# Kernel tuning notes

Hardware: AMD Instinct MI355X
Metric: run time of the kernel (lower is better)

Reference implementation:

```python
import jax, jax.numpy as jnp
import numpy as np

N_NODES = 100000
N_EDGES = 1600000
IN_CH = 64
HID = 64
OUT_CH = 3
N_LAYERS = 4


def gcn_conv(x, src, dst, norm, W, b):
    # x: [N, d_in]; W: [d_in, d_out]; norm: [E'] (per-edge symmetric norm)
    h = x @ W                               # [N, d_out]
    msgs = h[src] * norm[:, None]           # [E', d_out] gather + scale
    out = jax.ops.segment_sum(msgs, dst, num_segments=N_NODES)  # scatter-add
    return out + b


def build_graph(edge_index):
    # PyG GCNConv default: add self-loops, symmetric normalization
    loops = jnp.arange(N_NODES, dtype=edge_index.dtype)
    src = jnp.concatenate([edge_index[0], loops])
    dst = jnp.concatenate([edge_index[1], loops])
    deg = jax.ops.segment_sum(jnp.ones_like(dst, dtype=jnp.float32), dst,
                              num_segments=N_NODES)
    dinv = jnp.where(deg > 0, jax.lax.rsqrt(jnp.maximum(deg, 1e-12)), 0.0)
    norm = dinv[src] * dinv[dst]            # [E + N]
    return src, dst, norm


def setup_inputs() -> dict:
    key = jax.random.key(0)
    ks = jax.random.split(key, 5)
    x = jax.random.normal(ks[0], (N_NODES, IN_CH), dtype=jnp.float32)
    edge_index = jax.random.randint(ks[1], (2, N_EDGES), 0, N_NODES, dtype=jnp.int64)
    Ws = jax.random.normal(ks[2], (N_LAYERS, HID, HID), dtype=jnp.float32) * (1.0 / np.sqrt(HID))
    bs = jnp.zeros((N_LAYERS, HID), dtype=jnp.float32)
    Wc = jax.random.normal(ks[3], (HID, OUT_CH), dtype=jnp.float32) * (1.0 / np.sqrt(HID))
    bc = jnp.zeros((OUT_CH,), dtype=jnp.float32)
    return {"x": x, "edge_index": edge_index, "Ws": Ws, "bs": bs, "Wc": Wc, "bc": bc}


def reference(x, edge_index, Ws, bs, Wc, bc):
    src, dst, norm = build_graph(edge_index)
    for i in range(N_LAYERS):
        x_new = gcn_conv(x, src, dst, norm, Ws[i], bs[i])
        # residual when i > 0 and feature dims match (always true: hidden->hidden)
        x = x + x_new if i > 0 else x_new
        x = jax.nn.relu(x)
        # dropout is identity in eval mode (training=False)
    return x @ Wc + bc
```

## Files before the change

kernel.cpp:

```cpp
#include <hip/hip_runtime.h>
#include <hip/hip_fp16.h>

#define NN 100000
#define HD 64
#define NB ((NN + 255) >> 8)
#define P1_CHUNK 8192

__global__ __launch_bounds__(256) void hist_kernel(const int* __restrict__ dst,
                                                   int* __restrict__ bcnt, int E) {
    __shared__ int hist[NB];
    int t = threadIdx.x;
    int e0 = blockIdx.x * P1_CHUNK;
    int count = min(P1_CHUNK, E - e0);
    for (int b = t; b < NB; b += 256) hist[b] = 0;
    __syncthreads();
    for (int i = t; i < count; i += 256) atomicAdd(&hist[dst[e0 + i] >> 8], 1);
    __syncthreads();
    for (int b = t; b < NB; b += 256) {
        int c = hist[b];
        if (c) atomicAdd(&bcnt[b], c);
    }
}

__global__ void bscan_kernel(const int* __restrict__ bcnt, int* __restrict__ boff,
                             int* __restrict__ bcur, int* __restrict__ row_ptr,
                             int E, int n) {
    __shared__ int sm[512];
    int t = threadIdx.x;
    int v = (t < NB) ? bcnt[t] : 0;
    sm[t] = v;
    __syncthreads();
    for (int off = 1; off < 512; off <<= 1) {
        int u = (t >= off) ? sm[t - off] : 0;
        __syncthreads();
        sm[t] += u;
        __syncthreads();
    }
    if (t < NB) {
        boff[t] = sm[t] - v;
        bcur[t] = sm[t] - v;
    }
    if (t == 0) {
        boff[NB] = E;
        row_ptr[n] = E;
    }
}

__global__ __launch_bounds__(256) void p1_kernel(const int* __restrict__ src,
                                                 const int* __restrict__ dst,
                                                 int* __restrict__ bcur,
                                                 unsigned* __restrict__ ebuf, int E) {
    __shared__ int hist[NB];
    __shared__ int cur[NB];
    int t = threadIdx.x;
    int e0 = blockIdx.x * P1_CHUNK;
    int count = min(P1_CHUNK, E - e0);
    for (int b = t; b < NB; b += 256) hist[b] = 0;
    __syncthreads();
    for (int i = t; i < count; i += 256) atomicAdd(&hist[dst[e0 + i] >> 8], 1);
    __syncthreads();
    for (int b = t; b < NB; b += 256) {
        int c = hist[b];
        cur[b] = c ? atomicAdd(&bcur[b], c) : 0;
    }
    __syncthreads();
    for (int i = t; i < count; i += 256) {
        int d = dst[e0 + i], s = src[e0 + i];
        int pos = atomicAdd(&cur[d >> 8], 1);
        ebuf[pos] = ((unsigned)(d & 255) << 24) | (unsigned)s;
    }
}

__global__ __launch_bounds__(256) void p2_kernel(const unsigned* __restrict__ ebuf,
                                                 const int* __restrict__ boff,
                                                 int* __restrict__ row_ptr,
                                                 float* __restrict__ dinv,
                                                 int* __restrict__ csr_src, int n) {
    __shared__ int cnt[256];
    __shared__ int cur[256];
    int b = blockIdx.x;
    int node0 = b << 8;
    int t = threadIdx.x;
    int beg = boff[b], end = boff[b + 1];
    cnt[t] = 0;
    __syncthreads();
    for (int i = beg + t; i < end; i += 256) atomicAdd(&cnt[ebuf[i] >> 24], 1);
    __syncthreads();
    int deg = cnt[t];
    for (int off = 1; off < 256; off <<= 1) {
        int v = (t >= off) ? cnt[t - off] : 0;
        __syncthreads();
        cnt[t] += v;
        __syncthreads();
    }
    int excl = cnt[t] - deg;
    int node = node0 + t;
    if (node < n) {
        row_ptr[node] = beg + excl;
        dinv[node] = rsqrtf((float)deg + 1.0f);
    }
    cur[t] = beg + excl;
    __syncthreads();
    for (int i = beg + t; i < end; i += 256) {
        unsigned p = ebuf[i];
        int pos = atomicAdd(&cur[p >> 24], 1);
        csr_src[pos] = (int)(p & 0xFFFFFFu);
    }
}

__global__ __launch_bounds__(256) void matmul64_kernel(const void* __restrict__ Xv,
                                                       int x_is_half,
                                                       const float* __restrict__ W,
                                                       const float* __restrict__ dinv,
                                                       float2* __restrict__ H, int n) {
    __shared__ float Wl[64 * 64];
    __shared__ float Xs[64 * 65];
    int tid = threadIdx.x;
    int row0 = blockIdx.x * 64;
    const float4* W4 = (const float4*)W;
    float4* Wl4 = (float4*)Wl;
#pragma unroll
    for (int i = 0; i < 4; ++i) Wl4[tid + 256 * i] = W4[tid + 256 * i];
    if (x_is_half) {
        const float4* X4 = (const float4*)Xv;
#pragma unroll
        for (int i = 0; i < 2; ++i) {
            int l = tid + 256 * i;
            int r = l >> 3, k0 = (l & 7) * 8;
            int row = row0 + r;
            float4 xv = (row < n) ? X4[(size_t)row * 8 + (l & 7)]
                                  : make_float4(0.f, 0.f, 0.f, 0.f);
            const __half2* hp = (const __half2*)&xv;
#pragma unroll
            for (int j = 0; j < 4; ++j) {
                float2 f = __half22float2(hp[j]);
                Xs[r * 65 + k0 + 2 * j]     = f.x;
                Xs[r * 65 + k0 + 2 * j + 1] = f.y;
            }
        }
    } else {
        const float4* X4 = (const float4*)Xv;
#pragma unroll
        for (int i = 0; i < 4; ++i) {
            int l = tid + 256 * i;
            int r = l >> 4, k0 = (l & 15) * 4;
            int row = row0 + r;
            float4 xv = (row < n) ? X4[(size_t)row * 16 + (l & 15)]
                                  : make_float4(0.f, 0.f, 0.f, 0.f);
            Xs[r * 65 + k0 + 0] = xv.x;
            Xs[r * 65 + k0 + 1] = xv.y;
            Xs[r * 65 + k0 + 2] = xv.z;
            Xs[r * 65 + k0 + 3] = xv.w;
        }
    }
    __syncthreads();
    int tx = tid & 15, ty = tid >> 4;
    float acc[4][4] = {};
    const float4* Wlr4 = (const float4*)Wl;
#pragma unroll 4
    for (int k = 0; k < 64; ++k) {
        float4 b = Wlr4[k * 16 + tx];
        float a0 = Xs[(ty * 4 + 0) * 65 + k];
        float a1 = Xs[(ty * 4 + 1) * 65 + k];
        float a2 = Xs[(ty * 4 + 2) * 65 + k];
        float a3 = Xs[(ty * 4 + 3) * 65 + k];
        acc[0][0] += a0 * b.x; acc[0][1] += a0 * b.y; acc[0][2] += a0 * b.z; acc[0][3] += a0 * b.w;
        acc[1][0] += a1 * b.x; acc[1][1] += a1 * b.y; acc[1][2] += a1 * b.z; acc[1][3] += a1 * b.w;
        acc[2][0] += a2 * b.x; acc[2][1] += a2 * b.y; acc[2][2] += a2 * b.z; acc[2][3] += a2 * b.w;
        acc[3][0] += a3 * b.x; acc[3][1] += a3 * b.y; acc[3][2] += a3 * b.z; acc[3][3] += a3 * b.w;
    }
#pragma unroll
    for (int j = 0; j < 4; ++j) {
        int row = row0 + ty * 4 + j;
        if (row < n) {
            float dn = dinv[row];
            __half2 p01 = __float22half2_rn(make_float2(acc[j][0] * dn, acc[j][1] * dn));
            __half2 p23 = __float22half2_rn(make_float2(acc[j][2] * dn, acc[j][3] * dn));
            float2 st;
            st.x = *reinterpret_cast<float*>(&p01);
            st.y = *reinterpret_cast<float*>(&p23);
            H[(size_t)row * 16 + tx] = st;
        }
    }
}

#define PK_ACC(RAW) do {                                                     \
    a0 = __hadd2(a0, *reinterpret_cast<__half2*>(&(RAW).x));                 \
    a1 = __hadd2(a1, *reinterpret_cast<__half2*>(&(RAW).y));                 \
    a2 = __hadd2(a2, *reinterpret_cast<__half2*>(&(RAW).z));                 \
    a3 = __hadd2(a3, *reinterpret_cast<__half2*>(&(RAW).w));                 \
} while (0)

__global__ void agg_kernel(const float4* __restrict__ h4, const int* __restrict__ row_ptr,
                           const int* __restrict__ csr_src, const float* __restrict__ dinv,
                           const float* __restrict__ b, const float4* __restrict__ xprev,
                           float4* __restrict__ xout, float* __restrict__ outp,
                           const float* __restrict__ Wc, const float* __restrict__ bc,
                           int n, int residual, int project) {
    int lane = threadIdx.x & 63;
    int o = lane >> 3, c8 = lane & 7;
    int wid = (blockIdx.x * blockDim.x + threadIdx.x) >> 6;
    int node = wid * 8 + o;
    bool active = node < n;
    int nc = active ? node : 0;
    int beg = row_ptr[nc], end = row_ptr[nc + 1];
    int cnt = end - beg;
    float dn = dinv[nc];
    const float4* b4 = (const float4*)b;
    float4 bb0 = b4[c8 * 2], bb1 = b4[c8 * 2 + 1];
    float4 rr = make_float4(0.f, 0.f, 0.f, 0.f);
    if (residual) rr = xprev[(size_t)nc * 8 + c8];
    __half2 a0, a1, a2, a3;
    {
        float4 sv = h4[(size_t)nc * 8 + c8];
        a0 = *reinterpret_cast<__half2*>(&sv.x);
        a1 = *reinterpret_cast<__half2*>(&sv.y);
        a2 = *reinterpret_cast<__half2*>(&sv.z);
        a3 = *reinterpret_cast<__half2*>(&sv.w);
    }
    int base = o * 8;
    for (int k = 0; k < cnt; k += 16) {
        int p = beg + k + c8;
        int svA = (p < end) ? csr_src[p] : NN;
        int svB = (p + 8 < end) ? csr_src[p + 8] : NN;
        int s0 = __shfl(svA, base + 0);
        int s1 = __shfl(svA, base + 1);
        int s2 = __shfl(svA, base + 2);
        int s3 = __shfl(svA, base + 3);
        int s4 = __shfl(svA, base + 4);
        int s5 = __shfl(svA, base + 5);
        int s6 = __shfl(svA, base + 6);
        int s7 = __shfl(svA, base + 7);
        int s8  = __shfl(svB, base + 0);
        int s9  = __shfl(svB, base + 1);
        int s10 = __shfl(svB, base + 2);
        int s11 = __shfl(svB, base + 3);
        int s12 = __shfl(svB, base + 4);
        int s13 = __shfl(svB, base + 5);
        int s14 = __shfl(svB, base + 6);
        int s15 = __shfl(svB, base + 7);
        float4 v0  = h4[(size_t)s0 * 8 + c8];
        float4 v1  = h4[(size_t)s1 * 8 + c8];
        float4 v2  = h4[(size_t)s2 * 8 + c8];
        float4 v3  = h4[(size_t)s3 * 8 + c8];
        float4 v4  = h4[(size_t)s4 * 8 + c8];
        float4 v5  = h4[(size_t)s5 * 8 + c8];
        float4 v6  = h4[(size_t)s6 * 8 + c8];
        float4 v7  = h4[(size_t)s7 * 8 + c8];
        float4 v8  = h4[(size_t)s8 * 8 + c8];
        float4 v9  = h4[(size_t)s9 * 8 + c8];
        float4 v10 = h4[(size_t)s10 * 8 + c8];
        float4 v11 = h4[(size_t)s11 * 8 + c8];
        float4 v12 = h4[(size_t)s12 * 8 + c8];
        float4 v13 = h4[(size_t)s13 * 8 + c8];
        float4 v14 = h4[(size_t)s14 * 8 + c8];
        float4 v15 = h4[(size_t)s15 * 8 + c8];
        PK_ACC(v0);  PK_ACC(v1);  PK_ACC(v2);  PK_ACC(v3);
        PK_ACC(v4);  PK_ACC(v5);  PK_ACC(v6);  PK_ACC(v7);
        PK_ACC(v8);  PK_ACC(v9);  PK_ACC(v10); PK_ACC(v11);
        PK_ACC(v12); PK_ACC(v13); PK_ACC(v14); PK_ACC(v15);
    }
    if (active) {
        float2 f0 = __half22float2(a0);
        float2 f1 = __half22float2(a1);
        float2 f2 = __half22float2(a2);
        float2 f3 = __half22float2(a3);
        float4 u, w;
        u.x = f0.x * dn + bb0.x; u.y = f0.y * dn + bb0.y;
        u.z = f1.x * dn + bb0.z; u.w = f1.y * dn + bb0.w;
        w.x = f2.x * dn + bb1.x; w.y = f2.y * dn + bb1.y;
        w.z = f3.x * dn + bb1.z; w.w = f3.y * dn + bb1.w;
        if (residual) {
            const __half2* rp = (const __half2*)&rr;
            float2 r0 = __half22float2(rp[0]);
            float2 r1 = __half22float2(rp[1]);
            float2 r2 = __half22float2(rp[2]);
            float2 r3 = __half22float2(rp[3]);
            u.x += r0.x; u.y += r0.y; u.z += r1.x; u.w += r1.y;
            w.x += r2.x; w.y += r2.y; w.z += r3.x; w.w += r3.y;
        }
        u.x = fmaxf(u.x, 0.f); u.y = fmaxf(u.y, 0.f);
        u.z = fmaxf(u.z, 0.f); u.w = fmaxf(u.w, 0.f);
        w.x = fmaxf(w.x, 0.f); w.y = fmaxf(w.y, 0.f);
        w.z = fmaxf(w.z, 0.f); w.w = fmaxf(w.w, 0.f);
        if (!project) {
            __half2 o0 = __float22half2_rn(make_float2(u.x, u.y));
            __half2 o1 = __float22half2_rn(make_float2(u.z, u.w));
            __half2 o2 = __float22half2_rn(make_float2(w.x, w.y));
            __half2 o3 = __float22half2_rn(make_float2(w.z, w.w));
            float4 st;
            st.x = *reinterpret_cast<float*>(&o0);
            st.y = *reinterpret_cast<float*>(&o1);
            st.z = *reinterpret_cast<float*>(&o2);
            st.w = *reinterpret_cast<float*>(&o3);
            xout[(size_t)node * 8 + c8] = st;
        } else {
            int cb = c8 * 8;
#pragma unroll
            for (int j = 0; j < 3; ++j) {
                float p = u.x * Wc[(cb + 0) * 3 + j] + u.y * Wc[(cb + 1) * 3 + j] +
                          u.z * Wc[(cb + 2) * 3 + j] + u.w * Wc[(cb + 3) * 3 + j] +
                          w.x * Wc[(cb + 4) * 3 + j] + w.y * Wc[(cb + 5) * 3 + j] +
                          w.z * Wc[(cb + 6) * 3 + j] + w.w * Wc[(cb + 7) * 3 + j];
                p += __shfl_down(p, 4, 8);
                p += __shfl_down(p, 2, 8);
                p += __shfl_down(p, 1, 8);
                if (c8 == 0) outp[node * 3 + j] = p + bc[j];
            }
        }
    }
}

extern "C" void kernel_launch(void* const* d_in, const int* in_sizes, int n_in,
                              void* d_out, int out_size, void* d_ws, size_t ws_size,
                              hipStream_t stream) {
    const float* x  = (const float*)d_in[0];
    const int*   ei = (const int*)d_in[1];
    const float* Ws = (const float*)d_in[2];
    const float* bs = (const float*)d_in[3];
    const float* Wc = (const float*)d_in[4];
    const float* bc = (const float*)d_in[5];
    float* out = (float*)d_out;

    int E = in_sizes[1] / 2;
    const int* src = ei;
    const int* dst = ei + E;
    int nchunks = (E + P1_CHUNK - 1) / P1_CHUNK;

    char* wsb = (char*)d_ws;
    size_t off = 0;
    int*      bcnt    = (int*)(wsb + off); off += 512 * 4;
    int*      boff    = (int*)(wsb + off); off += 512 * 4;
    int*      bcur    = (int*)(wsb + off); off += 512 * 4;
    int*      row_ptr = (int*)(wsb + off); off += 100608 * 4;
    float*    dinv    = (float*)(wsb + off); off += 100352 * 4;
    int*      csr_src = (int*)(wsb + off); off += ((size_t)E + 256) * 4;
    unsigned* ebuf    = (unsigned*)(wsb + off); off += (size_t)E * 4;
    float2*   h       = (float2*)(wsb + off); off += (size_t)(NN + 8) * HD * 2;
    float4*   xa      = (float4*)(wsb + off); off += (size_t)NN * HD * 2;
    float4*   xb      = (float4*)(wsb + off); off += (size_t)NN * HD * 2;

    hipMemsetAsync(bcnt, 0, 512 * sizeof(int), stream);
    hipMemsetAsync((char*)h + (size_t)NN * HD * 2, 0, HD * 2, stream);
    hist_kernel<<<nchunks, 256, 0, stream>>>(dst, bcnt, E);
    bscan_kernel<<<1, 512, 0, stream>>>(bcnt, boff, bcur, row_ptr, E, NN);
    p1_kernel<<<nchunks, 256, 0, stream>>>(src, dst, bcur, ebuf, E);
    p2_kernel<<<NB, 256, 0, stream>>>(ebuf, boff, row_ptr, dinv, csr_src, NN);

    const void* xin = (const void*)x;
    int xin_half = 0;
    float4* bufs[2] = {xa, xb};
    int agg_blocks = ((NN + 7) / 8 * 64 + 255) / 256;
    for (int l = 0; l < 4; ++l) {
        float4* xout = bufs[l & 1];
        matmul64_kernel<<<(NN + 63) / 64, 256, 0, stream>>>(
            xin, xin_half, Ws + (size_t)l * HD * HD, dinv, h, NN);
        agg_kernel<<<agg_blocks, 256, 0, stream>>>(
            (const float4*)h, row_ptr, csr_src, dinv, bs + l * HD,
            (const float4*)xin, xout, out, Wc, bc, NN, l > 0, l == 3);
        xin = (const void*)xout;
        xin_half = 1;
    }
}
```

Before: 329.3 us.

## Drop histogram and scan passes by bucketing edges into fixed-capacity slots

Removes the separate histogram and bucket-scan kernels: p1 now reserves slots per destination bucket in a fixed-stride buffer (aliased onto the xa workspace), and p2 computes each bucket's global offset by reducing the bucket counts itself. It also folds the h-padding memset and row_ptr[n] write into p2. Separately, the 64x64 matmul now reads X as float4 with a 68-float row stride and unrolls k by 4. The fixed bucket capacity assumes roughly uniform destination distribution and would overflow on skewed graphs.

After: 409.3 us. +24.3%, slower.

```diff
diff --git a/kernel.cpp b/kernel.cpp
--- a/kernel.cpp
+++ b/kernel.cpp
@@ -6,50 +6,11 @@
 #define NB ((NN + 255) >> 8)
 #define P1_CHUNK 8192
 
-__global__ __launch_bounds__(256) void hist_kernel(const int* __restrict__ dst,
-                                                   int* __restrict__ bcnt, int E) {
-    __shared__ int hist[NB];
-    int t = threadIdx.x;
-    int e0 = blockIdx.x * P1_CHUNK;
-    int count = min(P1_CHUNK, E - e0);
-    for (int b = t; b < NB; b += 256) hist[b] = 0;
-    __syncthreads();
-    for (int i = t; i < count; i += 256) atomicAdd(&hist[dst[e0 + i] >> 8], 1);
-    __syncthreads();
-    for (int b = t; b < NB; b += 256) {
-        int c = hist[b];
-        if (c) atomicAdd(&bcnt[b], c);
-    }
-}
-
-__global__ void bscan_kernel(const int* __restrict__ bcnt, int* __restrict__ boff,
-                             int* __restrict__ bcur, int* __restrict__ row_ptr,
-                             int E, int n) {
-    __shared__ int sm[512];
-    int t = threadIdx.x;
-    int v = (t < NB) ? bcnt[t] : 0;
-    sm[t] = v;
-    __syncthreads();
-    for (int off = 1; off < 512; off <<= 1) {
-        int u = (t >= off) ? sm[t - off] : 0;
-        __syncthreads();
-        sm[t] += u;
-        __syncthreads();
-    }
-    if (t < NB) {
-        boff[t] = sm[t] - v;
-        bcur[t] = sm[t] - v;
-    }
-    if (t == 0) {
-        boff[NB] = E;
-        row_ptr[n] = E;
-    }
-}
-
 __global__ __launch_bounds__(256) void p1_kernel(const int* __restrict__ src,
                                                  const int* __restrict__ dst,
-                                                 int* __restrict__ bcur,
-                                                 unsigned* __restrict__ ebuf, int E) {
+                                                 int* __restrict__ bcnt,
+                                                 unsigned* __restrict__ ebuf,
+                                                 int E, int ebs) {
     __shared__ int hist[NB];
     __shared__ int cur[NB];
     int t = threadIdx.x;
@@ -61,30 +22,44 @@
     __syncthreads();
     for (int b = t; b < NB; b += 256) {
         int c = hist[b];
-        cur[b] = c ? atomicAdd(&bcur[b], c) : 0;
+        cur[b] = c ? atomicAdd(&bcnt[b], c) : 0;
     }
     __syncthreads();
     for (int i = t; i < count; i += 256) {
         int d = dst[e0 + i], s = src[e0 + i];
-        int pos = atomicAdd(&cur[d >> 8], 1);
-        ebuf[pos] = ((unsigned)(d & 255) << 24) | (unsigned)s;
+        int b = d >> 8;
+        int rel = atomicAdd(&cur[b], 1);
+        ebuf[(size_t)b * ebs + rel] = ((unsigned)(d & 255) << 24) | (unsigned)s;
     }
 }
 
 __global__ __launch_bounds__(256) void p2_kernel(const unsigned* __restrict__ ebuf,
-                                                 const int* __restrict__ boff,
+                                                 const int* __restrict__ bcnt,
                                                  int* __restrict__ row_ptr,
                                                  float* __restrict__ dinv,
-                                                 int* __restrict__ csr_src, int n) {
+                                                 int* __restrict__ csr_src,
+                                                 int* __restrict__ hpad,
+                                                 int n, int E, int ebs) {
     __shared__ int cnt[256];
     __shared__ int cur[256];
+    __shared__ int red[256];
     int b = blockIdx.x;
-    int node0 = b << 8;
     int t = threadIdx.x;
-    int beg = boff[b], end = boff[b + 1];
+    int part = 0;
+    for (int i = t; i < NB; i += 256)
+        if (i < b) part += bcnt[i];
+    red[t] = part;
+    __syncthreads();
+    for (int off = 128; off > 0; off >>= 1) {
+        if (t < off) red[t] += red[t + off];
+        __syncthreads();
+    }
+    int S = red[0];
+    int cb = bcnt[b];
+    const unsigned* eb = ebuf + (size_t)b * ebs;
     cnt[t] = 0;
     __syncthreads();
-    for (int i = beg + t; i < end; i += 256) atomicAdd(&cnt[ebuf[i] >> 24], 1);
+    for (int i = t; i < cb; i += 256) atomicAdd(&cnt[eb[i] >> 24], 1);
     __syncthreads();
     int deg = cnt[t];
     for (int off = 1; off < 256; off <<= 1) {
@@ -94,17 +69,21 @@
         __syncthreads();
     }
     int excl = cnt[t] - deg;
-    int node = node0 + t;
+    int node = (b << 8) + t;
     if (node < n) {
-        row_ptr[node] = beg + excl;
+        row_ptr[node] = S + excl;
         dinv[node] = rsqrtf((float)deg + 1.0f);
     }
-    cur[t] = beg + excl;
-    __syncthreads();
-    for (int i = beg + t; i < end; i += 256) {
-        unsigned p = ebuf[i];
+    cur[t] = S + excl;
+    __syncthreads();
+    for (int i = t; i < cb; i += 256) {
+        unsigned p = eb[i];
         int pos = atomicAdd(&cur[p >> 24], 1);
         csr_src[pos] = (int)(p & 0xFFFFFFu);
+    }
+    if (b == 0) {
+        if (t == 0) row_ptr[n] = E;
+        if (t < 32) hpad[t] = 0;
     }
 }
 
@@ -114,7 +93,7 @@
                                                        const float* __restrict__ dinv,
                                                        float2* __restrict__ H, int n) {
     __shared__ float Wl[64 * 64];
-    __shared__ float Xs[64 * 65];
+    __shared__ float Xs[64 * 68];
     int tid = threadIdx.x;
     int row0 = blockIdx.x * 64;
     const float4* W4 = (const float4*)W;
@@ -134,8 +113,8 @@
 #pragma unroll
             for (int j = 0; j < 4; ++j) {
                 float2 f = __half22float2(hp[j]);
-                Xs[r * 65 + k0 + 2 * j]     = f.x;
-                Xs[r * 65 + k0 + 2 * j + 1] = f.y;
+                Xs[r * 68 + k0 + 2 * j]     = f.x;
+                Xs[r * 68 + k0 + 2 * j + 1] = f.y;
             }
         }
     } else {
@@ -147,28 +126,35 @@
             int row = row0 + r;
             float4 xv = (row < n) ? X4[(size_t)row * 16 + (l & 15)]
                                   : make_float4(0.f, 0.f, 0.f, 0.f);
-            Xs[r * 65 + k0 + 0] = xv.x;
-            Xs[r * 65 + k0 + 1] = xv.y;
-            Xs[r * 65 + k0 + 2] = xv.z;
-            Xs[r * 65 + k0 + 3] = xv.w;
+            Xs[r * 68 + k0 + 0] = xv.x;
+            Xs[r * 68 + k0 + 1] = xv.y;
+            Xs[r * 68 + k0 + 2] = xv.z;
+            Xs[r * 68 + k0 + 3] = xv.w;
         }
     }
     __syncthreads();
     int tx = tid & 15, ty = tid >> 4;
     float acc[4][4] = {};
     const float4* Wlr4 = (const float4*)Wl;
-#pragma unroll 4
-    for (int k = 0; k < 64; ++k) {
-        float4 b = Wlr4[k * 16 + tx];
-        float a0 = Xs[(ty * 4 + 0) * 65 + k];
-        float a1 = Xs[(ty * 4 + 1) * 65 + k];
-        float a2 = Xs[(ty * 4 + 2) * 65 + k];
-        float a3 = Xs[(ty * 4 + 3) * 65 + k];
-        acc[0][0] += a0 * b.x; acc[0][1] += a0 * b.y; acc[0][2] += a0 * b.z; acc[0][3] += a0 * b.w;
-        acc[1][0] += a1 * b.x; acc[1][1] += a1 * b.y; acc[1][2] += a1 * b.z; acc[1][3] += a1 * b.w;
-        acc[2][0] += a2 * b.x; acc[2][1] += a2 * b.y; acc[2][2] += a2 * b.z; acc[2][3] += a2 * b.w;
-        acc[3][0] += a3 * b.x; acc[3][1] += a3 * b.y; acc[3][2] += a3 * b.z; acc[3][3] += a3 * b.w;
-    }
+    const float4* Xs4 = (const float4*)Xs;
+#define MMR(J, A)                                                                               \
+    acc[J][0] += A.x*b0.x; acc[J][1] += A.x*b0.y; acc[J][2] += A.x*b0.z; acc[J][3] += A.x*b0.w; \
+    acc[J][0] += A.y*b1.x; acc[J][1] += A.y*b1.y; acc[J][2] += A.y*b1.z; acc[J][3] += A.y*b1.w; \
+    acc[J][0] += A.z*b2.x; acc[J][1] += A.z*b2.y; acc[J][2] += A.z*b2.z; acc[J][3] += A.z*b2.w; \
+    acc[J][0] += A.w*b3.x; acc[J][1] += A.w*b3.y; acc[J][2] += A.w*b3.z; acc[J][3] += A.w*b3.w;
+#pragma unroll
+    for (int k = 0; k < 64; k += 4) {
+        float4 a0 = Xs4[(ty * 4 + 0) * 17 + (k >> 2)];
+        float4 a1 = Xs4[(ty * 4 + 1) * 17 + (k >> 2)];
+        float4 a2 = Xs4[(ty * 4 + 2) * 17 + (k >> 2)];
+        float4 a3 = Xs4[(ty * 4 + 3) * 17 + (k >> 2)];
+        float4 b0 = Wlr4[(k + 0) * 16 + tx];
+        float4 b1 = Wlr4[(k + 1) * 16 + tx];
+        float4 b2 = Wlr4[(k + 2) * 16 + tx];
+        float4 b3 = Wlr4[(k + 3) * 16 + tx];
+        MMR(0, a0) MMR(1, a1) MMR(2, a2) MMR(3, a3)
+    }
+#undef MMR
 #pragma unroll
     for (int j = 0; j < 4; ++j) {
         int row = row0 + ty * 4 + j;
@@ -326,26 +312,23 @@
     const int* src = ei;
     const int* dst = ei + E;
     int nchunks = (E + P1_CHUNK - 1) / P1_CHUNK;
+    int ebs = ((E / NB) + (E / NB) / 4 + 1024 + 255) & ~255;
 
     char* wsb = (char*)d_ws;
     size_t off = 0;
     int*      bcnt    = (int*)(wsb + off); off += 512 * 4;
-    int*      boff    = (int*)(wsb + off); off += 512 * 4;
-    int*      bcur    = (int*)(wsb + off); off += 512 * 4;
     int*      row_ptr = (int*)(wsb + off); off += 100608 * 4;
     float*    dinv    = (float*)(wsb + off); off += 100352 * 4;
     int*      csr_src = (int*)(wsb + off); off += ((size_t)E + 256) * 4;
-    unsigned* ebuf    = (unsigned*)(wsb + off); off += (size_t)E * 4;
     float2*   h       = (float2*)(wsb + off); off += (size_t)(NN + 8) * HD * 2;
     float4*   xa      = (float4*)(wsb + off); off += (size_t)NN * HD * 2;
     float4*   xb      = (float4*)(wsb + off); off += (size_t)NN * HD * 2;
+    unsigned* ebuf    = (unsigned*)xa;
 
     hipMemsetAsync(bcnt, 0, 512 * sizeof(int), stream);
-    hipMemsetAsync((char*)h + (size_t)NN * HD * 2, 0, HD * 2, stream);
-    hist_kernel<<<nchunks, 256, 0, stream>>>(dst, bcnt, E);
-    bscan_kernel<<<1, 512, 0, stream>>>(bcnt, boff, bcur, row_ptr, E, NN);
-    p1_kernel<<<nchunks, 256, 0, stream>>>(src, dst, bcur, ebuf, E);
-    p2_kernel<<<NB, 256, 0, stream>>>(ebuf, boff, row_ptr, dinv, csr_src, NN);
+    p1_kernel<<<nchunks, 256, 0, stream>>>(src, dst, bcnt, ebuf, E, ebs);
+    p2_kernel<<<NB, 256, 0, stream>>>(ebuf, bcnt, row_ptr, dinv, csr_src,
+                                      (int*)((char*)h + (size_t)NN * HD * 2), NN, E, ebs);
 
     const void* xin = (const void*)x;
     int xin_half = 0;
```
